# Performance work log

Measured on AMD Instinct MI355X. Metric: run time of the kernel, lower is better.

## Reference

```python
import jax, jax.numpy as jnp
import numpy as np

B, S, HID, H, DB = 4, 2048, 512, 8, 8
DH = HID // H  # head dim = 64


def setup_inputs() -> dict:
    key = jax.random.key(0)
    ks = jax.random.split(key, 14)
    s = 0.02
    return {
        "q": jax.random.normal(ks[0], (B, S, HID), jnp.float32),
        "k": jax.random.normal(ks[1], (B, S, HID), jnp.float32),
        "v": jax.random.normal(ks[2], (B, S, HID), jnp.float32),
        "attn_bias": jax.random.normal(ks[3], (B, S, S, DB), jnp.float32),
        "Wq": jax.random.normal(ks[4], (HID, HID), jnp.float32) * s,
        "bq": jnp.zeros((HID,), jnp.float32),
        "Wk": jax.random.normal(ks[5], (HID, HID), jnp.float32) * s,
        "bk": jnp.zeros((HID,), jnp.float32),
        "Wv": jax.random.normal(ks[6], (HID, HID), jnp.float32) * s,
        "bv": jnp.zeros((HID,), jnp.float32),
        "Wb": jax.random.normal(ks[7], (H, DB), jnp.float32) * s,
        "bb": jnp.zeros((H,), jnp.float32),
        "Wo": jax.random.normal(ks[8], (HID, HID), jnp.float32) * s,
        "bo": jnp.zeros((HID,), jnp.float32),
    }


def reference(q, k, v, attn_bias, Wq, bq, Wk, bk, Wv, bv, Wb, bb, Wo, bo):
    scale = DH ** (-0.5)
    # projections: torch Linear is x @ W.T + b
    qh = (q @ Wq.T + bq).reshape(B, S, H, DH).transpose(0, 2, 1, 3)  # [B,H,S,D]
    kh = (k @ Wk.T + bk).reshape(B, S, H, DH).transpose(0, 2, 1, 3)
    vh = (v @ Wv.T + bv).reshape(B, S, H, DH).transpose(0, 2, 1, 3)
    scores = jnp.einsum("bhqd,bhkd->bhqk", qh * scale, kh)  # [B,H,S,S]
    bias = (attn_bias @ Wb.T + bb).transpose(0, 3, 1, 2)  # [B,H,S,S]
    attn = jax.nn.softmax(scores + bias, axis=-1)
    out = jnp.einsum("bhqk,bhkd->bhqd", attn, vh)  # [B,H,S,D]
    out = out.transpose(0, 2, 1, 3).reshape(B, S, HID)
    return out @ Wo.T + bo
```

## Files before the change

### kernel.cpp

```cpp
#include <hip/hip_runtime.h>
#include <cstdint>
#include <cstddef>

#define BB 4
#define SS 2048
#define HIDD 512
#define HH 8
#define DHH 64
#define DBB 8

typedef __attribute__((ext_vector_type(4))) float f32x4;
typedef __attribute__((ext_vector_type(8))) short s16x8;
typedef __attribute__((ext_vector_type(4))) short s16x4;

__device__ __forceinline__ short f2bf(float x) {
  unsigned u = __builtin_bit_cast(unsigned, x);
  u += 0x7FFFu + ((u >> 16) & 1u);
  return (short)(u >> 16);
}
__device__ __forceinline__ float bf2f(short s) {
  unsigned u = ((unsigned)(unsigned short)s) << 16;
  return __builtin_bit_cast(float, u);
}

template <int MODE>
__global__ __launch_bounds__(256) void gemm_xwT(const float* __restrict__ X,
                                                const float* __restrict__ W,
                                                const float* __restrict__ bias,
                                                float* __restrict__ outF,
                                                short* __restrict__ outB) {
  __shared__ short xs[64][40];
  __shared__ short wsh[64][40];
  const int tid = threadIdx.x;
  const int wave = tid >> 6, lane = tid & 63;
  const int quad = lane >> 4, m16 = lane & 15;
  const int m0 = blockIdx.x * 64, n0 = blockIdx.y * 64;
  const int wm = (wave & 1) * 32, wn = (wave >> 1) * 32;

  f32x4 acc[2][2];
#pragma unroll
  for (int a = 0; a < 2; a++)
#pragma unroll
    for (int b2 = 0; b2 < 2; b2++) acc[a][b2] = (f32x4){0.f, 0.f, 0.f, 0.f};

  for (int k0 = 0; k0 < HIDD; k0 += 32) {
#pragma unroll
    for (int i = 0; i < 2; i++) {
      int c = tid + i * 256;
      int row = c >> 3, kc = c & 7;
      f32x4 xv = *(const f32x4*)(X + (size_t)(m0 + row) * HIDD + k0 + kc * 4);
      f32x4 wv = *(const f32x4*)(W + (size_t)(n0 + row) * HIDD + k0 + kc * 4);
      s16x4 xb, wb2;
#pragma unroll
      for (int j = 0; j < 4; j++) { xb[j] = f2bf(xv[j]); wb2[j] = f2bf(wv[j]); }
      *(s16x4*)(&xs[row][kc * 4]) = xb;
      *(s16x4*)(&wsh[row][kc * 4]) = wb2;
    }
    __syncthreads();
    s16x8 af[2], bfr[2];
    af[0] = *(const s16x8*)(&xs[wm + m16][quad * 8]);
    af[1] = *(const s16x8*)(&xs[wm + 16 + m16][quad * 8]);
    bfr[0] = *(const s16x8*)(&wsh[wn + m16][quad * 8]);
    bfr[1] = *(const s16x8*)(&wsh[wn + 16 + m16][quad * 8]);
    acc[0][0] = __builtin_amdgcn_mfma_f32_16x16x32_bf16(af[0], bfr[0], acc[0][0], 0, 0, 0);
    acc[0][1] = __builtin_amdgcn_mfma_f32_16x16x32_bf16(af[0], bfr[1], acc[0][1], 0, 0, 0);
    acc[1][0] = __builtin_amdgcn_mfma_f32_16x16x32_bf16(af[1], bfr[0], acc[1][0], 0, 0, 0);
    acc[1][1] = __builtin_amdgcn_mfma_f32_16x16x32_bf16(af[1], bfr[1], acc[1][1], 0, 0, 0);
    __syncthreads();
  }

#pragma unroll
  for (int a = 0; a < 2; a++)
#pragma unroll
    for (int b2 = 0; b2 < 2; b2++)
#pragma unroll
      for (int r = 0; r < 4; r++) {
        int m = m0 + wm + a * 16 + quad * 4 + r;
        int n = n0 + wn + b2 * 16 + m16;
        float val = acc[a][b2][r] + bias[n];
        if (MODE == 0) {
          int b_ = m >> 11, s = m & 2047, h = n >> 6, d = n & 63;
          outB[((size_t)(b_ * HH + h) * SS + s) * DHH + d] = f2bf(val * 0.125f);
        } else if (MODE == 1) {
          int b_ = m >> 11, s = m & 2047, h = n >> 6, d = n & 63;
          outB[((size_t)(b_ * HH + h) * SS + s) * DHH + d] = f2bf(val);
        } else if (MODE == 2) {
          int b_ = m >> 11, s = m & 2047, h = n >> 6, d = n & 63;
          outB[((size_t)(b_ * HH + h) * DHH + d) * SS + s] = f2bf(val);
        } else {
          outF[(size_t)m * HIDD + n] = val;
        }
      }
}

__global__ __launch_bounds__(512) void flash_attn(const short* __restrict__ qh,
                                                  const short* __restrict__ kh,
                                                  const short* __restrict__ vh,
                                                  const float* __restrict__ attn_bias,
                                                  const float* __restrict__ Wb,
                                                  const float* __restrict__ bb,
                                                  float* __restrict__ attn_out) {
  __shared__ short kv[20480];
  __shared__ short bp[HH][16][34];
  __shared__ short pbuf[8][16][40];
  __shared__ float wbs[72];

  const int tid = threadIdx.x;
  const int wave = tid >> 6, lane = tid & 63;
  const int quad = lane >> 4, m16 = lane & 15;
  const int b = blockIdx.x >> 7;
  const int q0 = (blockIdx.x & 127) << 4;
  const int h = wave;

  if (tid < 72) wbs[tid] = (tid < 64) ? Wb[tid] : bb[tid - 64];

  const size_t qoff = ((size_t)((b * HH + h) * SS) + q0 + m16) * DHH;
  s16x8 qf0 = *(const s16x8*)(qh + qoff + quad * 8);
  s16x8 qf1 = *(const s16x8*)(qh + qoff + 32 + quad * 8);

  f32x4 oacc[4];
#pragma unroll
  for (int dt = 0; dt < 4; dt++) oacc[dt] = (f32x4){0.f, 0.f, 0.f, 0.f};
  float m_r[4], l_r[4];
#pragma unroll
  for (int r = 0; r < 4; r++) { m_r[r] = -3.0e38f; l_r[r] = 0.f; }

  __syncthreads();

  for (int k0 = 0; k0 < SS; k0 += 32) {
#pragma unroll
    for (int i = 0; i < 4; i++) {
      int c = tid + i * 512;
      int key = c >> 6, rest = c & 63;
      int hh2 = rest >> 3, dc = rest & 7;
      s16x8 val = *(const s16x8*)(kh + ((size_t)((b * HH + hh2) * SS) + k0 + key) * DHH + dc * 8);
      *(s16x8*)(&kv[key * 520 + hh2 * 64 + dc * 8]) = val;
    }
    {
      int ql = tid >> 5, kl = tid & 31;
      const float* bptr = attn_bias + ((size_t)(b * SS + q0 + ql) * SS + k0 + kl) * DBB;
      f32x4 b0 = *(const f32x4*)(bptr);
      f32x4 b1 = *(const f32x4*)(bptr + 4);
#pragma unroll
      for (int h2 = 0; h2 < 8; h2++) {
        float a2 = wbs[64 + h2];
#pragma unroll
        for (int d = 0; d < 4; d++) {
          a2 += b0[d] * wbs[h2 * 8 + d];
          a2 += b1[d] * wbs[h2 * 8 + 4 + d];
        }
        bp[h2][ql][kl] = f2bf(a2);
      }
    }
    __syncthreads();

    f32x4 sc[2];
#pragma unroll
    for (int nt = 0; nt < 2; nt++) {
      s16x8 kf0 = *(const s16x8*)(&kv[(nt * 16 + m16) * 520 + h * 64 + quad * 8]);
      s16x8 kf1 = *(const s16x8*)(&kv[(nt * 16 + m16) * 520 + h * 64 + 32 + quad * 8]);
      f32x4 z = (f32x4){0.f, 0.f, 0.f, 0.f};
      z = __builtin_amdgcn_mfma_f32_16x16x32_bf16(qf0, kf0, z, 0, 0, 0);
      z = __builtin_amdgcn_mfma_f32_16x16x32_bf16(qf1, kf1, z, 0, 0, 0);
      sc[nt] = z;
    }

#pragma unroll
    for (int r = 0; r < 4; r++) {
      int row = quad * 4 + r;
      float s0 = sc[0][r] + bf2f(bp[h][row][m16]);
      float s1 = sc[1][r] + bf2f(bp[h][row][16 + m16]);
      float v = fmaxf(s0, s1);
      v = fmaxf(v, __shfl_xor(v, 1, 16));
      v = fmaxf(v, __shfl_xor(v, 2, 16));
      v = fmaxf(v, __shfl_xor(v, 4, 16));
      v = fmaxf(v, __shfl_xor(v, 8, 16));
      float nm = fmaxf(m_r[r], v);
      float al = __expf(m_r[r] - nm);
      m_r[r] = nm;
      float p0 = __expf(s0 - nm);
      float p1 = __expf(s1 - nm);
      float rs = p0 + p1;
      rs += __shfl_xor(rs, 1, 16);
      rs += __shfl_xor(rs, 2, 16);
      rs += __shfl_xor(rs, 4, 16);
      rs += __shfl_xor(rs, 8, 16);
      l_r[r] = l_r[r] * al + rs;
#pragma unroll
      for (int dt = 0; dt < 4; dt++) oacc[dt][r] *= al;
      pbuf[wave][row][m16] = f2bf(p0);
      pbuf[wave][row][16 + m16] = f2bf(p1);
    }
    __syncthreads();

#pragma unroll
    for (int i = 0; i < 4; i++) {
      int c = tid + i * 512;
      int d = c >> 2, kc = c & 3;
      s16x8 val = *(const s16x8*)(vh + ((size_t)((b * HH + (d >> 6)) * DHH + (d & 63)) * SS) + k0 + kc * 8);
      *(s16x8*)(&kv[d * 40 + kc * 8]) = val;
    }
    __syncthreads();

    s16x8 pf = *(const s16x8*)(&pbuf[wave][m16][quad * 8]);
#pragma unroll
    for (int dt = 0; dt < 4; dt++) {
      s16x8 vf = *(const s16x8*)(&kv[(h * 64 + dt * 16 + m16) * 40 + quad * 8]);
      oacc[dt] = __builtin_amdgcn_mfma_f32_16x16x32_bf16(pf, vf, oacc[dt], 0, 0, 0);
    }
    __syncthreads();
  }

#pragma unroll
  for (int dt = 0; dt < 4; dt++)
#pragma unroll
    for (int r = 0; r < 4; r++) {
      float val = oacc[dt][r] / l_r[r];
      attn_out[(size_t)(b * SS + q0 + quad * 4 + r) * HIDD + h * 64 + dt * 16 + m16] = val;
    }
}

extern "C" void kernel_launch(void* const* d_in, const int* in_sizes, int n_in,
                              void* d_out, int out_size, void* d_ws, size_t ws_size,
                              hipStream_t stream) {
  const float* q = (const float*)d_in[0];
  const float* k = (const float*)d_in[1];
  const float* v = (const float*)d_in[2];
  const float* attn_bias = (const float*)d_in[3];
  const float* Wq = (const float*)d_in[4];
  const float* bq = (const float*)d_in[5];
  const float* Wk = (const float*)d_in[6];
  const float* bk = (const float*)d_in[7];
  const float* Wv = (const float*)d_in[8];
  const float* bv = (const float*)d_in[9];
  const float* Wb = (const float*)d_in[10];
  const float* bb = (const float*)d_in[11];
  const float* Wo = (const float*)d_in[12];
  const float* bo = (const float*)d_in[13];
  float* out = (float*)d_out;

  short* qh = (short*)d_ws;
  short* kh = qh + (size_t)4194304;
  short* vh = kh + (size_t)4194304;
  float* attn_ws = (float*)(vh + (size_t)4194304);

  dim3 g(128, 8), blk(256);
  gemm_xwT<0><<<g, blk, 0, stream>>>(q, Wq, bq, nullptr, qh);
  gemm_xwT<1><<<g, blk, 0, stream>>>(k, Wk, bk, nullptr, kh);
  gemm_xwT<2><<<g, blk, 0, stream>>>(v, Wv, bv, nullptr, vh);
  flash_attn<<<512, 512, 0, stream>>>(qh, kh, vh, attn_bias, Wb, bb, attn_ws);
  gemm_xwT<3><<<g, blk, 0, stream>>>(attn_ws, Wo, bo, out, nullptr);
}
```

Before: 1.031 ms.

## Rework GEMMs and flash attention with bias prefetch, direct K/V loads, bf16 intermediates

```diff
diff --git a/kernel.cpp b/kernel.cpp
--- a/kernel.cpp
+++ b/kernel.cpp
@@ -24,99 +24,123 @@
 }
 
 template <int MODE>
-__global__ __launch_bounds__(256) void gemm_xwT(const float* __restrict__ X,
+__global__ __launch_bounds__(512, 4) void gemm2(const float* __restrict__ Xf,
+                                                const short* __restrict__ Xb,
                                                 const float* __restrict__ W,
                                                 const float* __restrict__ bias,
                                                 float* __restrict__ outF,
                                                 short* __restrict__ outB) {
-  __shared__ short xs[64][40];
-  __shared__ short wsh[64][40];
+  __shared__ short As[128][72];
+  __shared__ short Bs[64][72];
   const int tid = threadIdx.x;
   const int wave = tid >> 6, lane = tid & 63;
   const int quad = lane >> 4, m16 = lane & 15;
-  const int m0 = blockIdx.x * 64, n0 = blockIdx.y * 64;
-  const int wm = (wave & 1) * 32, wn = (wave >> 1) * 32;
-
-  f32x4 acc[2][2];
-#pragma unroll
-  for (int a = 0; a < 2; a++)
-#pragma unroll
-    for (int b2 = 0; b2 < 2; b2++) acc[a][b2] = (f32x4){0.f, 0.f, 0.f, 0.f};
-
-  for (int k0 = 0; k0 < HIDD; k0 += 32) {
-#pragma unroll
-    for (int i = 0; i < 2; i++) {
-      int c = tid + i * 256;
-      int row = c >> 3, kc = c & 7;
-      f32x4 xv = *(const f32x4*)(X + (size_t)(m0 + row) * HIDD + k0 + kc * 4);
-      f32x4 wv = *(const f32x4*)(W + (size_t)(n0 + row) * HIDD + k0 + kc * 4);
-      s16x4 xb, wb2;
-#pragma unroll
-      for (int j = 0; j < 4; j++) { xb[j] = f2bf(xv[j]); wb2[j] = f2bf(wv[j]); }
-      *(s16x4*)(&xs[row][kc * 4]) = xb;
-      *(s16x4*)(&wsh[row][kc * 4]) = wb2;
+  const int m0 = blockIdx.y * 128, n0 = blockIdx.x * 64;
+  const int wm = (wave & 1) * 64, wn = (wave >> 1) * 16;
+
+  f32x4 acc[4];
+#pragma unroll
+  for (int a = 0; a < 4; a++) acc[a] = (f32x4){0.f, 0.f, 0.f, 0.f};
+
+  const int xrow = tid >> 2, xcb = (tid & 3) * 16;
+  const int wrow = tid >> 3, wcb = (tid & 7) * 8;
+
+  for (int k0 = 0; k0 < HIDD; k0 += 64) {
+    if (MODE == 3) {
+      s16x8 x0 = *(const s16x8*)(Xb + (size_t)(m0 + xrow) * HIDD + k0 + xcb);
+      s16x8 x1 = *(const s16x8*)(Xb + (size_t)(m0 + xrow) * HIDD + k0 + xcb + 8);
+      *(s16x8*)(&As[xrow][xcb]) = x0;
+      *(s16x8*)(&As[xrow][xcb + 8]) = x1;
+    } else {
+      const float* xp = Xf + (size_t)(m0 + xrow) * HIDD + k0 + xcb;
+      f32x4 xv[4];
+#pragma unroll
+      for (int i = 0; i < 4; i++) xv[i] = *(const f32x4*)(xp + i * 4);
+      s16x8 pk0, pk1;
+#pragma unroll
+      for (int j = 0; j < 4; j++) { pk0[j] = f2bf(xv[0][j]); pk0[4 + j] = f2bf(xv[1][j]); }
+#pragma unroll
+      for (int j = 0; j < 4; j++) { pk1[j] = f2bf(xv[2][j]); pk1[4 + j] = f2bf(xv[3][j]); }
+      *(s16x8*)(&As[xrow][xcb]) = pk0;
+      *(s16x8*)(&As[xrow][xcb + 8]) = pk1;
+    }
+    {
+      const float* wp = W + (size_t)(n0 + wrow) * HIDD + k0 + wcb;
+      f32x4 w0 = *(const f32x4*)(wp);
+      f32x4 w1 = *(const f32x4*)(wp + 4);
+      s16x8 pk;
+#pragma unroll
+      for (int j = 0; j < 4; j++) { pk[j] = f2bf(w0[j]); pk[4 + j] = f2bf(w1[j]); }
+      *(s16x8*)(&Bs[wrow][wcb]) = pk;
     }
     __syncthreads();
-    s16x8 af[2], bfr[2];
-    af[0] = *(const s16x8*)(&xs[wm + m16][quad * 8]);
-    af[1] = *(const s16x8*)(&xs[wm + 16 + m16][quad * 8]);
-    bfr[0] = *(const s16x8*)(&wsh[wn + m16][quad * 8]);
-    bfr[1] = *(const s16x8*)(&wsh[wn + 16 + m16][quad * 8]);
-    acc[0][0] = __builtin_amdgcn_mfma_f32_16x16x32_bf16(af[0], bfr[0], acc[0][0], 0, 0, 0);
-    acc[0][1] = __builtin_amdgcn_mfma_f32_16x16x32_bf16(af[0], bfr[1], acc[0][1], 0, 0, 0);
-    acc[1][0] = __builtin_amdgcn_mfma_f32_16x16x32_bf16(af[1], bfr[0], acc[1][0], 0, 0, 0);
-    acc[1][1] = __builtin_amdgcn_mfma_f32_16x16x32_bf16(af[1], bfr[1], acc[1][1], 0, 0, 0);
+#pragma unroll
+    for (int kc = 0; kc < 2; kc++) {
+      s16x8 bf = *(const s16x8*)(&Bs[wn + m16][kc * 32 + quad * 8]);
+#pragma unroll
+      for (int a = 0; a < 4; a++) {
+        s16x8 af = *(const s16x8*)(&As[wm + a * 16 + m16][kc * 32 + quad * 8]);
+        acc[a] = __builtin_amdgcn_mfma_f32_16x16x32_bf16(af, bf, acc[a], 0, 0, 0);
+      }
+    }
     __syncthreads();
   }
 
-#pragma unroll
-  for (int a = 0; a < 2; a++)
-#pragma unroll
-    for (int b2 = 0; b2 < 2; b2++)
+  const int n = n0 + wn + m16;
+  const float bn = bias[n];
+#pragma unroll
+  for (int a = 0; a < 4; a++) {
+    const int mb = m0 + wm + a * 16 + quad * 4;
+    if (MODE == 2) {
+      int b_ = mb >> 11, s = mb & 2047, h = n >> 6, d = n & 63;
+      s16x4 pk;
+#pragma unroll
+      for (int r = 0; r < 4; r++) pk[r] = f2bf(acc[a][r] + bn);
+      *(s16x4*)(outB + ((size_t)(b_ * HH + h) * DHH + d) * SS + s) = pk;
+    } else {
 #pragma unroll
       for (int r = 0; r < 4; r++) {
-        int m = m0 + wm + a * 16 + quad * 4 + r;
-        int n = n0 + wn + b2 * 16 + m16;
-        float val = acc[a][b2][r] + bias[n];
+        int m = mb + r;
+        float val = acc[a][r] + bn;
         if (MODE == 0) {
           int b_ = m >> 11, s = m & 2047, h = n >> 6, d = n & 63;
           outB[((size_t)(b_ * HH + h) * SS + s) * DHH + d] = f2bf(val * 0.125f);
         } else if (MODE == 1) {
           int b_ = m >> 11, s = m & 2047, h = n >> 6, d = n & 63;
           outB[((size_t)(b_ * HH + h) * SS + s) * DHH + d] = f2bf(val);
-        } else if (MODE == 2) {
-          int b_ = m >> 11, s = m & 2047, h = n >> 6, d = n & 63;
-          outB[((size_t)(b_ * HH + h) * DHH + d) * SS + s] = f2bf(val);
         } else {
           outF[(size_t)m * HIDD + n] = val;
         }
       }
-}
-
-__global__ __launch_bounds__(512) void flash_attn(const short* __restrict__ qh,
-                                                  const short* __restrict__ kh,
-                                                  const short* __restrict__ vh,
-                                                  const float* __restrict__ attn_bias,
-                                                  const float* __restrict__ Wb,
-                                                  const float* __restrict__ bb,
-                                                  float* __restrict__ attn_out) {
-  __shared__ short kv[20480];
-  __shared__ short bp[HH][16][34];
-  __shared__ short pbuf[8][16][40];
+    }
+  }
+}
+
+__global__ __launch_bounds__(512, 4) void flash_attn(const short* __restrict__ qh,
+                                                     const short* __restrict__ kh,
+                                                     const short* __restrict__ vh,
+                                                     const float* __restrict__ attn_bias,
+                                                     const float* __restrict__ Wb,
+                                                     const float* __restrict__ bb,
+                                                     short* __restrict__ attn_out) {
+  __shared__ short bp[2][HH][16][68];
+  __shared__ short pbuf[HH][16][76];
   __shared__ float wbs[72];
 
   const int tid = threadIdx.x;
   const int wave = tid >> 6, lane = tid & 63;
   const int quad = lane >> 4, m16 = lane & 15;
-  const int b = blockIdx.x >> 7;
-  const int q0 = (blockIdx.x & 127) << 4;
   const int h = wave;
+  const int j = blockIdx.x;
+  const int b = (j & 7) >> 1;
+  const int w = ((j >> 3) << 1) | (j & 1);
+  const int q0 = w << 4;
 
   if (tid < 72) wbs[tid] = (tid < 64) ? Wb[tid] : bb[tid - 64];
 
   const size_t qoff = ((size_t)((b * HH + h) * SS) + q0 + m16) * DHH;
-  s16x8 qf0 = *(const s16x8*)(qh + qoff + quad * 8);
-  s16x8 qf1 = *(const s16x8*)(qh + qoff + 32 + quad * 8);
+  const s16x8 qf0 = *(const s16x8*)(qh + qoff + quad * 8);
+  const s16x8 qf1 = *(const s16x8*)(qh + qoff + 32 + quad * 8);
 
   f32x4 oacc[4];
 #pragma unroll
@@ -125,40 +149,53 @@
 #pragma unroll
   for (int r = 0; r < 4; r++) { m_r[r] = -3.0e38f; l_r[r] = 0.f; }
 
+  const int ql = tid >> 5, kc2 = (tid & 31) * 2;
+  const float* bbase = attn_bias + ((size_t)(b * SS + q0 + ql) * SS + kc2) * DBB;
+
+  f32x4 pre[4];
+#pragma unroll
+  for (int i = 0; i < 4; i++)
+    pre[i] = __builtin_nontemporal_load((const f32x4*)(bbase) + i);
+
+  const size_t khb = (size_t)((b * HH + h) * SS) * DHH;
+  const size_t vhb = (size_t)((b * HH + h) * DHH) * SS;
+
   __syncthreads();
 
-  for (int k0 = 0; k0 < SS; k0 += 32) {
-#pragma unroll
-    for (int i = 0; i < 4; i++) {
-      int c = tid + i * 512;
-      int key = c >> 6, rest = c & 63;
-      int hh2 = rest >> 3, dc = rest & 7;
-      s16x8 val = *(const s16x8*)(kh + ((size_t)((b * HH + hh2) * SS) + k0 + key) * DHH + dc * 8);
-      *(s16x8*)(&kv[key * 520 + hh2 * 64 + dc * 8]) = val;
-    }
+  for (int it = 0; it < 32; ++it) {
+    const int buf = it & 1;
+    const int k0 = it * 64;
+
+#pragma unroll
+    for (int h2 = 0; h2 < HH; h2++) {
+      float a0 = wbs[64 + h2], a1 = a0;
+#pragma unroll
+      for (int d = 0; d < 4; d++) {
+        a0 += pre[0][d] * wbs[h2 * 8 + d];
+        a0 += pre[1][d] * wbs[h2 * 8 + 4 + d];
+        a1 += pre[2][d] * wbs[h2 * 8 + d];
+        a1 += pre[3][d] * wbs[h2 * 8 + 4 + d];
+      }
+      unsigned pk = (unsigned)(unsigned short)f2bf(a0) |
+                    ((unsigned)(unsigned short)f2bf(a1) << 16);
+      *(unsigned*)(&bp[buf][h2][ql][kc2]) = pk;
+    }
+    __syncthreads();
+
     {
-      int ql = tid >> 5, kl = tid & 31;
-      const float* bptr = attn_bias + ((size_t)(b * SS + q0 + ql) * SS + k0 + kl) * DBB;
-      f32x4 b0 = *(const f32x4*)(bptr);
-      f32x4 b1 = *(const f32x4*)(bptr + 4);
-#pragma unroll
-      for (int h2 = 0; h2 < 8; h2++) {
-        float a2 = wbs[64 + h2];
-#pragma unroll
-        for (int d = 0; d < 4; d++) {
-          a2 += b0[d] * wbs[h2 * 8 + d];
-          a2 += b1[d] * wbs[h2 * 8 + 4 + d];
-        }
-        bp[h2][ql][kl] = f2bf(a2);
-      }
-    }
-    __syncthreads();
-
-    f32x4 sc[2];
-#pragma unroll
-    for (int nt = 0; nt < 2; nt++) {
-      s16x8 kf0 = *(const s16x8*)(&kv[(nt * 16 + m16) * 520 + h * 64 + quad * 8]);
-      s16x8 kf1 = *(const s16x8*)(&kv[(nt * 16 + m16) * 520 + h * 64 + 32 + quad * 8]);
+      const int kn = (it < 31) ? (it + 1) * 64 : it * 64;
+      const float* nb = bbase + (size_t)kn * DBB;
+#pragma unroll
+      for (int i = 0; i < 4; i++)
+        pre[i] = __builtin_nontemporal_load((const f32x4*)(nb) + i);
+    }
+
+    f32x4 sc[4];
+#pragma unroll
+    for (int nt = 0; nt < 4; nt++) {
+      const short* kp = kh + khb + (size_t)(k0 + nt * 16 + m16) * DHH;
+      s16x8 kf0 = *(const s16x8*)(kp + quad * 8);
+      s16x8 kf1 = *(const s16x8*)(kp + 32 + quad * 8);
       f32x4 z = (f32x4){0.f, 0.f, 0.f, 0.f};
       z = __builtin_amdgcn_mfma_f32_16x16x32_bf16(qf0, kf0, z, 0, 0, 0);
       z = __builtin_amdgcn_mfma_f32_16x16x32_bf16(qf1, kf1, z, 0, 0, 0);
@@ -167,20 +204,22 @@
 
 #pragma unroll
     for (int r = 0; r < 4; r++) {
-      int row = quad * 4 + r;
-      float s0 = sc[0][r] + bf2f(bp[h][row][m16]);
-      float s1 = sc[1][r] + bf2f(bp[h][row][16 + m16]);
-      float v = fmaxf(s0, s1);
+      const int row = quad * 4 + r;
+      float s0 = sc[0][r] + bf2f(bp[buf][h][row][m16]);
+      float s1 = sc[1][r] + bf2f(bp[buf][h][row][16 + m16]);
+      float s2 = sc[2][r] + bf2f(bp[buf][h][row][32 + m16]);
+      float s3 = sc[3][r] + bf2f(bp[buf][h][row][48 + m16]);
+      float v = fmaxf(fmaxf(s0, s1), fmaxf(s2, s3));
       v = fmaxf(v, __shfl_xor(v, 1, 16));
       v = fmaxf(v, __shfl_xor(v, 2, 16));
       v = fmaxf(v, __shfl_xor(v, 4, 16));
       v = fmaxf(v, __shfl_xor(v, 8, 16));
-      float nm = fmaxf(m_r[r], v);
-      float al = __expf(m_r[r] - nm);
+      const float nm = fmaxf(m_r[r], v);
+      const float al = __expf(m_r[r] - nm);
       m_r[r] = nm;
-      float p0 = __expf(s0 - nm);
-      float p1 = __expf(s1 - nm);
-      float rs = p0 + p1;
+      float p0 = __expf(s0 - nm), p1 = __expf(s1 - nm);
+      float p2 = __expf(s2 - nm), p3 = __expf(s3 - nm);
+      float rs = (p0 + p1) + (p2 + p3);
       rs += __shfl_xor(rs, 1, 16);
       rs += __shfl_xor(rs, 2, 16);
       rs += __shfl_xor(rs, 4, 16);
@@ -188,27 +227,22 @@
       l_r[r] = l_r[r] * al + rs;
 #pragma unroll
       for (int dt = 0; dt < 4; dt++) oacc[dt][r] *= al;
-      pbuf[wave][row][m16] = f2bf(p0);
-      pbuf[wave][row][16 + m16] = f2bf(p1);
-    }
-    __syncthreads();
-
-#pragma unroll
-    for (int i = 0; i < 4; i++) {
-      int c = tid + i * 512;
-      int d = c >> 2, kc = c & 3;
-      s16x8 val = *(const s16x8*)(vh + ((size_t)((b * HH + (d >> 6)) * DHH + (d & 63)) * SS) + k0 + kc * 8);
-      *(s16x8*)(&kv[d * 40 + kc * 8]) = val;
-    }
-    __syncthreads();
-
-    s16x8 pf = *(const s16x8*)(&pbuf[wave][m16][quad * 8]);
+      pbuf[h][row][m16] = f2bf(p0);
+      pbuf[h][row][16 + m16] = f2bf(p1);
+      pbuf[h][row][32 + m16] = f2bf(p2);
+      pbuf[h][row][48 + m16] = f2bf(p3);
+    }
+
+    const s16x8 pf0 = *(const s16x8*)(&pbuf[h][m16][quad * 8]);
+    const s16x8 pf1 = *(const s16x8*)(&pbuf[h][m16][32 + quad * 8]);
 #pragma unroll
     for (int dt = 0; dt < 4; dt++) {
-      s16x8 vf = *(const s16x8*)(&kv[(h * 64 + dt * 16 + m16) * 40 + quad * 8]);
-      oacc[dt] = __builtin_amdgcn_mfma_f32_16x16x32_bf16(pf, vf, oacc[dt], 0, 0, 0);
-    }
-    __syncthreads();
+      const short* vp = vh + vhb + (size_t)(dt * 16 + m16) * SS + k0;
+      s16x8 vf0 = *(const s16x8*)(vp + quad * 8);
+      s16x8 vf1 = *(const s16x8*)(vp + 32 + quad * 8);
+      oacc[dt] = __builtin_amdgcn_mfma_f32_16x16x32_bf16(pf0, vf0, oacc[dt], 0, 0, 0);
+      oacc[dt] = __builtin_amdgcn_mfma_f32_16x16x32_bf16(pf1, vf1, oacc[dt], 0, 0, 0);
+    }
   }
 
 #pragma unroll
@@ -216,7 +250,7 @@
 #pragma unroll
     for (int r = 0; r < 4; r++) {
       float val = oacc[dt][r] / l_r[r];
-      attn_out[(size_t)(b * SS + q0 + quad * 4 + r) * HIDD + h * 64 + dt * 16 + m16] = val;
+      attn_out[(size_t)(b * SS + q0 + quad * 4 + r) * HIDD + h * DHH + dt * 16 + m16] = f2bf(val);
     }
 }
 
@@ -241,13 +275,13 @@
 
   short* qh = (short*)d_ws;
   short* kh = qh + (size_t)4194304;
-  short* vh = kh + (size_t)4194304;
-  float* attn_ws = (float*)(vh + (size_t)4194304);
-
-  dim3 g(128, 8), blk(256);
-  gemm_xwT<0><<<g, blk, 0, stream>>>(q, Wq, bq, nullptr, qh);
-  gemm_xwT<1><<<g, blk, 0, stream>>>(k, Wk, bk, nullptr, kh);
-  gemm_xwT<2><<<g, blk, 0, stream>>>(v, Wv, bv, nullptr, vh);
-  flash_attn<<<512, 512, 0, stream>>>(qh, kh, vh, attn_bias, Wb, bb, attn_ws);
-  gemm_xwT<3><<<g, blk, 0, stream>>>(attn_ws, Wo, bo, out, nullptr);
-}
+  short* vhT = kh + (size_t)4194304;
+  short* attn_b = vhT + (size_t)4194304;
+
+  dim3 g(8, 64), blk(512);
+  gemm2<0><<<g, blk, 0, stream>>>(q, nullptr, Wq, bq, nullptr, qh);
+  gemm2<1><<<g, blk, 0, stream>>>(k, nullptr, Wk, bk, nullptr, kh);
+  gemm2<2><<<g, blk, 0, stream>>>(v, nullptr, Wv, bv, nullptr, vhT);
+  flash_attn<<<512, blk, 0, stream>>>(qh, kh, vhT, attn_bias, Wb, bb, attn_b);
+  gemm2<3><<<g, blk, 0, stream>>>(nullptr, attn_b, Wo, bo, out, nullptr);
+}
```

Result: no change. 1.041 ms (+1.0%).
